# Optimization experiments

Measured on AMD Instinct MI355X. Metric: run time of the kernel, lower is better.

Reference implementation:

```python
import jax, jax.numpy as jnp
import numpy as np

B, T, D = 8, 16384, 128


def setup_inputs() -> dict:
    key = jax.random.key(0)
    ks = jax.random.split(key, 14)
    sc = lambda fan_in: 1.0 / np.sqrt(fan_in)
    x = jax.random.normal(ks[0], (B, T, D), jnp.float32)
    return {
        "x": x,
        # BindingField (scale 0): bind_key / bind_query Linear(D, D//2)
        "Wk": jax.random.normal(ks[1], (D, D // 2), jnp.float32) * sc(D),
        "bk": jnp.zeros((D // 2,), jnp.float32),
        "Wq": jax.random.normal(ks[2], (D, D // 2), jnp.float32) * sc(D),
        "bq": jnp.zeros((D // 2,), jnp.float32),
        # aggregator (scale 0): Linear(D,D) -> LayerNorm(D) -> ReLU -> Linear(D,D)
        "Wa1": jax.random.normal(ks[3], (D, D), jnp.float32) * sc(D),
        "ba1": jnp.zeros((D,), jnp.float32),
        "ln_g": jnp.ones((D,), jnp.float32),
        "ln_b": jnp.zeros((D,), jnp.float32),
        "Wa2": jax.random.normal(ks[4], (D, D), jnp.float32) * sc(D),
        "ba2": jnp.zeros((D,), jnp.float32),
        # downward_influence (scale 0): Linear(D,D)
        "Wd": jax.random.normal(ks[5], (D, D), jnp.float32) * sc(D),
        "bd": jnp.zeros((D,), jnp.float32),
    }


def reference(x, Wk, bk, Wq, bq, Wa1, ba1, ln_g, ln_b, Wa2, ba2, Wd, bd):
    Bn, Tn, Dn = x.shape
    BIND_THRESHOLD = 0.5
    LN_EPS = 1e-5

    # ---- BindingField: binding strength between adjacent tokens ----
    keys = x[:, :-1] @ Wk + bk                       # [B, T-1, D/2]
    queries = x[:, 1:] @ Wq + bq                     # [B, T-1, D/2]
    strength = jax.nn.sigmoid((keys * queries).sum(-1) / float(np.sqrt(Dn // 2)))
    bind = strength > BIND_THRESHOLD                 # [B, T-1]

    # chunk_starts: token 0 always starts; token t starts iff NOT bound to t-1
    chunk_starts = jnp.concatenate([jnp.ones((Bn, 1), bool), ~bind], axis=1)
    seg = jnp.cumsum(chunk_starts.astype(jnp.int32), axis=1) - 1  # [B, T] chunk id per token

    # ---- aggregate_chunks: ragged mean-pool via segment_sum (pad to T chunk slots) ----
    seg_flat = (seg + jnp.arange(Bn, dtype=jnp.int32)[:, None] * Tn).reshape(-1)
    sums = jax.ops.segment_sum(x.reshape(-1, Dn), seg_flat, num_segments=Bn * Tn)
    counts = jax.ops.segment_sum(jnp.ones((Bn * Tn,), x.dtype), seg_flat,
                                 num_segments=Bn * Tn)
    chunk_mean = (sums / jnp.maximum(counts, 1.0)[:, None]).reshape(Bn, Tn, Dn)

    # aggregator MLP: Linear -> LayerNorm -> ReLU -> Linear
    h = chunk_mean @ Wa1 + ba1
    mu = h.mean(-1, keepdims=True)
    var = ((h - mu) ** 2).mean(-1, keepdims=True)    # biased var, as torch LayerNorm
    h = (h - mu) * jax.lax.rsqrt(var + LN_EPS) * ln_g + ln_b
    agg = jax.nn.relu(h) @ Wa2 + ba2                 # [B, T(chunk slots), D]

    # ---- apply_downward_influence: broadcast chunk signal back to its tokens ----
    infl = agg @ Wd + bd                             # [B, T(chunks), D]
    gathered = jnp.take_along_axis(infl, seg[..., None].astype(jnp.int32), axis=1)
    gate = jax.nn.sigmoid(gathered)
    return x * gate + x
```

## Files before the change

kernel.cpp:

```cpp
#include <hip/hip_runtime.h>
#include <math.h>

#define BB 8
#define TT 16384
#define DD 128
#define DH 64
#define FCAP 32768
#define FMARGIN 0.05f

typedef _Float16 half8 __attribute__((ext_vector_type(8)));
typedef float f32x4 __attribute__((ext_vector_type(4)));

union H8 { half8 h; uint4 q; ushort us[8]; };

static __device__ __forceinline__ float4 ld4(const float* p) { return *(const float4*)p; }

static __device__ __forceinline__ uint pk2(float a, float b) {
    union { _Float16 f; ushort u; } A, B;
    A.f = (_Float16)a; B.f = (_Float16)b;
    return (uint)A.u | ((uint)B.u << 16);
}

static __device__ __forceinline__ void split8h(const float4 v0, const float4 v1,
                                               half8* xh, half8* xl)
{
    float f[8] = {v0.x, v0.y, v0.z, v0.w, v1.x, v1.y, v1.z, v1.w};
    half8 h, l;
    #pragma unroll
    for (int j = 0; j < 8; ++j) {
        _Float16 hv = (_Float16)f[j];
        h[j] = hv;
        l[j] = (_Float16)(f[j] - (float)hv);
    }
    *xh = h; *xl = l;
}

__global__ __launch_bounds__(64) void k_wprep(
    const float* __restrict__ Wa1, const float* __restrict__ Wa2,
    const float* __restrict__ Wd, const float* __restrict__ Wk,
    const float* __restrict__ Wq, ushort* __restrict__ wfm,
    ushort* __restrict__ wfb, int* __restrict__ fcnt)
{
    const int l  = threadIdx.x;
    const int nt = blockIdx.x & 7;
    const int kb = blockIdx.x >> 3;
    const int ly = blockIdx.y;
    if (ly == 0 && blockIdx.x == 0 && l == 0) *fcnt = 0;
    const int n  = nt * 16 + (l & 15);
    const int k0 = kb * 32 + (l >> 4) * 8;
    H8 v;
    if (ly < 3) {
        const float* W = (ly == 0) ? Wa1 : (ly == 1) ? Wa2 : Wd;
        #pragma unroll
        for (int e = 0; e < 8; ++e) v.h[e] = (_Float16)W[(k0 + e) * DD + n];
        *(uint4*)(wfm + (size_t)(((ly * 8 + nt) * 4 + kb) * 64 + l) * 8) = v.q;
    } else {
        #pragma unroll
        for (int e = 0; e < 8; ++e) {
            float w = (n < 64) ? Wk[(k0 + e) * DH + n] : Wq[(k0 + e) * DH + n - 64];
            v.h[e] = (_Float16)w;
        }
        *(uint4*)(wfb + (size_t)((nt * 4 + kb) * 64 + l) * 8) = v.q;
    }
}

__global__ __launch_bounds__(256, 2) void k_bind(
    const float* __restrict__ x, const ushort* __restrict__ wfb,
    const float* __restrict__ bk, const float* __restrict__ bq,
    int* __restrict__ cstart, int* __restrict__ flist, int* __restrict__ fcnt)
{
    __shared__ uint4 Bs4[2048];
    __shared__ float bnd[4][64];
    const int b    = blockIdx.y;
    const int tb   = blockIdx.x * 64;
    const int tid  = threadIdx.x;
    const int wv   = tid >> 6;
    const int l    = tid & 63;
    const int lo16 = l & 15;
    const int g    = l >> 4;

    {
        const uint4* wsrc = (const uint4*)wfb;
        #pragma unroll
        for (int j = 0; j < 8; ++j) { int idx = tid + j * 256; Bs4[idx] = wsrc[idx]; }
    }

    const float* xrow = x + ((size_t)b * TT + tb + wv * 16 + lo16) * DD;
    half8 xh[4], xl[4];
    #pragma unroll
    for (int kb = 0; kb < 4; ++kb) {
        float4 v0 = ld4(xrow + kb * 32 + g * 8);
        float4 v1 = ld4(xrow + kb * 32 + g * 8 + 4);
        split8h(v0, v1, &xh[kb], &xl[kb]);
    }
    int r64 = tb + 64; if (r64 > TT - 1) r64 = TT - 1;
    const float* xq = x + ((size_t)b * TT + r64) * DD;
    half8 qh[4], ql[4];
    H8 z; z.q.x = z.q.y = z.q.z = z.q.w = 0u;
    #pragma unroll
    for (int kb = 0; kb < 4; ++kb) {
        qh[kb] = z.h; ql[kb] = z.h;
        if (lo16 == 0) {
            float4 v0 = ld4(xq + kb * 32 + g * 8);
            float4 v1 = ld4(xq + kb * 32 + g * 8 + 4);
            split8h(v0, v1, &qh[kb], &ql[kb]);
        }
    }

    f32x4 acc[8];
    #pragma unroll
    for (int nt = 0; nt < 8; ++nt) {
        int col = nt * 16 + lo16;
        float bias = (col < 64) ? bk[col] : bq[col - 64];
        acc[nt] = (f32x4){bias, bias, bias, bias};
    }
    f32x4 acc4;
    {
        float bias = bq[wv * 16 + lo16];
        acc4 = (f32x4){bias, bias, bias, bias};
    }

    __syncthreads();
    const ushort* Bs = (const ushort*)Bs4;
    const ushort* Bs_halo = Bs + (size_t)((4 + wv) * 4 * 64 + l) * 8;
    #pragma unroll
    for (int kb = 0; kb < 4; ++kb) {
        half8 bh[8];
        #pragma unroll
        for (int nt = 0; nt < 8; ++nt)
            bh[nt] = *(const half8*)(Bs + (size_t)((nt * 4 + kb) * 64 + l) * 8);
        #pragma unroll
        for (int nt = 0; nt < 8; ++nt) {
            acc[nt] = __builtin_amdgcn_mfma_f32_16x16x32_f16(xh[kb], bh[nt], acc[nt], 0, 0, 0);
            acc[nt] = __builtin_amdgcn_mfma_f32_16x16x32_f16(xl[kb], bh[nt], acc[nt], 0, 0, 0);
        }
        half8 bh4 = *(const half8*)(Bs_halo + (size_t)kb * 64 * 8);
        acc4 = __builtin_amdgcn_mfma_f32_16x16x32_f16(qh[kb], bh4, acc4, 0, 0, 0);
        acc4 = __builtin_amdgcn_mfma_f32_16x16x32_f16(ql[kb], bh4, acc4, 0, 0, 0);
    }

    if (l < 16) {
        if (wv > 0) {
            #pragma unroll
            for (int nt = 0; nt < 4; ++nt) bnd[wv - 1][nt * 16 + lo16] = acc[4 + nt][0];
        }
        bnd[3][wv * 16 + lo16] = acc4[0];
    }
    __syncthreads();

    float qn3[4];
    #pragma unroll
    for (int nt = 0; nt < 4; ++nt) qn3[nt] = __shfl_down(acc[4 + nt][0], 16);
    if (g == 3) {
        #pragma unroll
        for (int nt = 0; nt < 4; ++nt) qn3[nt] = bnd[wv][nt * 16 + lo16];
    }
    float s[4];
    #pragma unroll
    for (int i = 0; i < 3; ++i) {
        float t = 0.f;
        #pragma unroll
        for (int nt = 0; nt < 4; ++nt) t += acc[nt][i] * acc[4 + nt][i + 1];
        s[i] = t;
    }
    {
        float t = 0.f;
        #pragma unroll
        for (int nt = 0; nt < 4; ++nt) t += acc[nt][3] * qn3[nt];
        s[3] = t;
    }
    #pragma unroll
    for (int i = 0; i < 4; ++i) {
        #pragma unroll
        for (int m = 1; m < 16; m <<= 1) s[i] += __shfl_xor(s[i], m);
    }
    if (lo16 == 0) {
        #pragma unroll
        for (int i = 0; i < 4; ++i) {
            int t = tb + wv * 16 + g * 4 + i;
            if (t <= TT - 2) {
                cstart[b * TT + t + 1] = (s[i] > 0.f) ? 0 : 1;
                if (fabsf(s[i]) < FMARGIN) {
                    int pos = atomicAdd(fcnt, 1);
                    if (pos < FCAP) flist[pos] = b * TT + t;
                }
            }
        }
    }
    if (blockIdx.x == 0 && tid == 0) cstart[b * TT] = 1;
}

__global__ __launch_bounds__(256) void k_fixup(
    const float* __restrict__ x, const float* __restrict__ Wk, const float* __restrict__ bk,
    const float* __restrict__ Wq, const float* __restrict__ bq,
    const int* __restrict__ flist, const int* __restrict__ fcnt, int* __restrict__ cstart)
{
    const int n    = min(*fcnt, FCAP);
    const int wv   = (blockIdx.x * 256 + threadIdx.x) >> 6;
    const int lane = threadIdx.x & 63;
    const int nwv  = gridDim.x * 4;
    for (int i = wv; i < n; i += nwv) {
        int idx = flist[i];
        int b = idx >> 14;
        int t = idx & (TT - 1);
        const float* xt = x + ((size_t)b * TT + t) * DD;
        float K = bk[lane], Q = bq[lane];
        #pragma unroll 8
        for (int k = 0; k < DD; ++k) {
            K = fmaf(xt[k],      Wk[k * DH + lane], K);
            Q = fmaf(xt[DD + k], Wq[k * DH + lane], Q);
        }
        float p = K * Q;
        #pragma unroll
        for (int m = 1; m < 64; m <<= 1) p += __shfl_xor(p, m);
        if (lane == 0) cstart[b * TT + t + 1] = (p > 0.f) ? 0 : 1;
    }
}

__global__ __launch_bounds__(1024) void k_scan(const int* __restrict__ cstart,
    int* __restrict__ seg, int* __restrict__ cs, int* __restrict__ numC)
{
    __shared__ int wsum[16];
    const int b = blockIdx.x, tid = threadIdx.x;
    const int wv = tid >> 6, lane = tid & 63;
    const int base = b * TT + tid * 16;
    int v[16];
    #pragma unroll
    for (int i = 0; i < 4; ++i) {
        int4 q = *(const int4*)(cstart + base + i * 4);
        v[i * 4 + 0] = q.x; v[i * 4 + 1] = q.y; v[i * 4 + 2] = q.z; v[i * 4 + 3] = q.w;
    }
    int s[16]; int run = 0;
    #pragma unroll
    for (int i = 0; i < 16; ++i) { run += v[i]; s[i] = run; }
    int incl = run;
    #pragma unroll
    for (int off = 1; off < 64; off <<= 1) {
        int t = __shfl_up(incl, off);
        if (lane >= off) incl += t;
    }
    if (lane == 63) wsum[wv] = incl;
    __syncthreads();
    if (tid < 16) {
        int w = wsum[tid];
        #pragma unroll
        for (int off = 1; off < 16; off <<= 1) {
            int t = __shfl_up(w, off, 16);
            if (tid >= off) w += t;
        }
        wsum[tid] = w;
    }
    __syncthreads();
    const int excl = (wv ? wsum[wv - 1] : 0) + incl - run;
    #pragma unroll
    for (int i = 0; i < 16; ++i) {
        int sg = excl + s[i] - 1;
        seg[base + i] = sg;
        if (v[i]) cs[b * (TT + 1) + sg] = tid * 16 + i;
    }
    if (tid == 1023) {
        int tot = excl + run;
        numC[b] = tot;
        cs[b * (TT + 1) + tot] = TT;
    }
}

__device__ __forceinline__ void mlp_gemm(f32x4 acc[8], const uint4* Afr4,
    const ushort* Bs, int wv, int l)
{
    half8 af[4];
    #pragma unroll
    for (int kb = 0; kb < 4; ++kb)
        af[kb] = *(const half8*)((const char*)Afr4 + ((wv * 4 + kb) * 64 + l) * 16);
    #pragma unroll
    for (int kb = 0; kb < 4; ++kb) {
        half8 bh[8];
        #pragma unroll
        for (int nt = 0; nt < 8; ++nt)
            bh[nt] = *(const half8*)(Bs + (size_t)((nt * 4 + kb) * 64 + l) * 8);
        #pragma unroll
        for (int nt = 0; nt < 8; ++nt)
            acc[nt] = __builtin_amdgcn_mfma_f32_16x16x32_f16(af[kb], bh[nt], acc[nt], 0, 0, 0);
    }
}

__global__ __launch_bounds__(256, 2) void k_mlp(
    const float* __restrict__ x, const int* __restrict__ cs,
    const float* __restrict__ ba1, const float* __restrict__ ln_g, const float* __restrict__ ln_b,
    const float* __restrict__ ba2, const float* __restrict__ bd,
    const ushort* __restrict__ wfm, const int* __restrict__ numC, float* __restrict__ cm)
{
    __shared__ union {
        float Tok[64 * 132];
        struct { uint4 Afr[1024]; uint4 Bs[2048]; } fb;
    } sm;
    const int b  = blockIdx.y;
    const int nC = numC[b];
    const int c0 = blockIdx.x * 64;
    if (c0 >= nC) return;
    const int tid  = threadIdx.x;
    const int wv   = tid >> 6;
    const int l    = tid & 63;
    const int lo16 = l & 15;
    const int g    = l >> 4;
    const ushort* Bs = (const ushort*)sm.fb.Bs;
    const uint4* wsrc = (const uint4*)wfm;

    const int cbase = b * (TT + 1);
    const int T0 = cs[cbase + c0];
    const int cEnd = (c0 + 64 < nC) ? (c0 + 64) : nC;
    const int T1 = cs[cbase + cEnd];
    int t0r[8], t1r[8];
    #pragma unroll
    for (int ii = 0; ii < 8; ++ii) {
        int r = (tid + ii * 256) >> 5;
        int c = c0 + r;
        t0r[ii] = (c < nC) ? cs[cbase + c] : 0;
        t1r[ii] = (c < nC) ? cs[cbase + c + 1] : 0;
    }
    float4 vals[8];
    #pragma unroll
    for (int ii = 0; ii < 8; ++ii) vals[ii] = make_float4(0.f, 0.f, 0.f, 0.f);

    for (int tt = T0; tt < T1; tt += 64) {
        __syncthreads();
        const int tEnd = (tt + 64 < T1) ? (tt + 64) : T1;
        for (int j = tid; j < (tEnd - tt) * 32; j += 256) {
            int trow = j >> 5, c4 = (j & 31) * 4;
            *(float4*)&sm.Tok[trow * 132 + c4] =
                ld4(x + ((size_t)b * TT + tt + trow) * DD + c4);
        }
        __syncthreads();
        #pragma unroll
        for (int ii = 0; ii < 8; ++ii) {
            int c4 = ((tid + ii * 256) & 31) * 4;
            int lo = (t0r[ii] > tt)   ? t0r[ii] : tt;
            int hi = (t1r[ii] < tEnd) ? t1r[ii] : tEnd;
            for (int t = lo; t < hi; ++t) {
                const float* ap = &sm.Tok[(t - tt) * 132 + c4];
                vals[ii].x += ap[0]; vals[ii].y += ap[1];
                vals[ii].z += ap[2]; vals[ii].w += ap[3];
            }
        }
    }
    __syncthreads();

    #pragma unroll
    for (int ii = 0; ii < 8; ++ii) {
        int i = tid + ii * 256;
        int r = i >> 5, c4 = (i & 31) * 4;
        float4 sv = make_float4(0.f, 0.f, 0.f, 0.f);
        if (c0 + r < nC) {
            float inv = 1.f / (float)(t1r[ii] - t0r[ii]);
            sv.x = vals[ii].x * inv; sv.y = vals[ii].y * inv;
            sv.z = vals[ii].z * inv; sv.w = vals[ii].w * inv;
        }
        int frag = (r >> 4) * 4 + (c4 >> 5);
        int lanef = (r & 15) + (((c4 & 31) >> 3) * 16);
        uint2 pk = make_uint2(pk2(sv.x, sv.y), pk2(sv.z, sv.w));
        *(uint2*)((char*)sm.fb.Afr + frag * 1024 + lanef * 16 + (c4 & 7) * 2) = pk;
    }
    #pragma unroll
    for (int j = 0; j < 8; ++j) { int idx = tid + j * 256; sm.fb.Bs[idx] = wsrc[idx]; }
    __syncthreads();

    f32x4 acc[8];
    #pragma unroll
    for (int nt = 0; nt < 8; ++nt) {
        float bias = ba1[nt * 16 + lo16];
        acc[nt] = (f32x4){bias, bias, bias, bias};
    }
    mlp_gemm(acc, sm.fb.Afr, Bs, wv, l);

    float mu_[4], rs_[4];
    #pragma unroll
    for (int i = 0; i < 4; ++i) {
        float smv = 0.f;
        #pragma unroll
        for (int nt = 0; nt < 8; ++nt) smv += acc[nt][i];
        #pragma unroll
        for (int k = 1; k < 16; k <<= 1) smv += __shfl_xor(smv, k, 16);
        mu_[i] = smv * (1.f / 128.f);
        float vs = 0.f;
        #pragma unroll
        for (int nt = 0; nt < 8; ++nt) { float d = acc[nt][i] - mu_[i]; vs += d * d; }
        #pragma unroll
        for (int k = 1; k < 16; k <<= 1) vs += __shfl_xor(vs, k, 16);
        rs_[i] = rsqrtf(vs * (1.f / 128.f) + 1e-5f);
    }
    float gam[8], bet[8];
    #pragma unroll
    for (int nt = 0; nt < 8; ++nt) { gam[nt] = ln_g[nt * 16 + lo16]; bet[nt] = ln_b[nt * 16 + lo16]; }

    __syncthreads();
    #pragma unroll
    for (int nt = 0; nt < 8; ++nt) {
        int cw = nt * 16 + lo16;
        int frag = wv * 4 + (cw >> 5);
        int lnf  = (((cw & 31) >> 3) * 16);
        #pragma unroll
        for (int i = 0; i < 4; ++i) {
            float h = fmaf((acc[nt][i] - mu_[i]) * rs_[i], gam[nt], bet[nt]);
            union { _Float16 f; ushort u; } cv; cv.f = (_Float16)fmaxf(h, 0.f);
            *((ushort*)((char*)sm.fb.Afr + frag * 1024 + ((g * 4 + i) + lnf) * 16 + (cw & 7) * 2)) = cv.u;
        }
    }
    #pragma unroll
    for (int j = 0; j < 8; ++j) { int idx = tid + j * 256; sm.fb.Bs[idx] = wsrc[2048 + idx]; }
    __syncthreads();

    #pragma unroll
    for (int nt = 0; nt < 8; ++nt) {
        float bias = ba2[nt * 16 + lo16];
        acc[nt] = (f32x4){bias, bias, bias, bias};
    }
    mlp_gemm(acc, sm.fb.Afr, Bs, wv, l);
    __syncthreads();
    #pragma unroll
    for (int nt = 0; nt < 8; ++nt) {
        int cw = nt * 16 + lo16;
        int frag = wv * 4 + (cw >> 5);
        int lnf  = (((cw & 31) >> 3) * 16);
        #pragma unroll
        for (int i = 0; i < 4; ++i) {
            union { _Float16 f; ushort u; } cv; cv.f = (_Float16)acc[nt][i];
            *((ushort*)((char*)sm.fb.Afr + frag * 1024 + ((g * 4 + i) + lnf) * 16 + (cw & 7) * 2)) = cv.u;
        }
    }
    #pragma unroll
    for (int j = 0; j < 8; ++j) { int idx = tid + j * 256; sm.fb.Bs[idx] = wsrc[4096 + idx]; }
    __syncthreads();

    #pragma unroll
    for (int nt = 0; nt < 8; ++nt) {
        float bias = bd[nt * 16 + lo16];
        acc[nt] = (f32x4){bias, bias, bias, bias};
    }
    mlp_gemm(acc, sm.fb.Afr, Bs, wv, l);
    #pragma unroll
    for (int i = 0; i < 4; ++i) {
        int row = c0 + wv * 16 + g * 4 + i;
        if (row < nC) {
            float* dst = cm + ((size_t)b * TT + row) * DD + lo16;
            #pragma unroll
            for (int nt = 0; nt < 8; ++nt)
                dst[nt * 16] = 1.f / (1.f + __expf(-acc[nt][i]));
        }
    }
}

__global__ __launch_bounds__(256) void k_out(const float* __restrict__ x,
    const int* __restrict__ seg, const float* __restrict__ gate, float* __restrict__ out)
{
    const size_t idx = (size_t)blockIdx.x * 256 + threadIdx.x;
    const size_t tok = idx >> 5;
    const int d4 = (int)(idx & 31);
    const int b  = (int)(tok >> 14);
    const int sg = seg[tok];
    float4 gv = ld4(gate + (((size_t)b << 14) + sg) * DD + d4 * 4);
    float4 xv = ld4(x + tok * DD + (size_t)d4 * 4);
    float4 o;
    o.x = fmaf(xv.x, gv.x, xv.x);
    o.y = fmaf(xv.y, gv.y, xv.y);
    o.z = fmaf(xv.z, gv.z, xv.z);
    o.w = fmaf(xv.w, gv.w, xv.w);
    *(float4*)(out + idx * 4) = o;
}

extern "C" void kernel_launch(void* const* d_in, const int* in_sizes, int n_in,
                              void* d_out, int out_size, void* d_ws, size_t ws_size,
                              hipStream_t stream)
{
    (void)in_sizes; (void)n_in; (void)out_size; (void)ws_size;
    const float* x    = (const float*)d_in[0];
    const float* Wk   = (const float*)d_in[1];
    const float* bk   = (const float*)d_in[2];
    const float* Wq   = (const float*)d_in[3];
    const float* bq   = (const float*)d_in[4];
    const float* Wa1  = (const float*)d_in[5];
    const float* ba1  = (const float*)d_in[6];
    const float* ln_g = (const float*)d_in[7];
    const float* ln_b = (const float*)d_in[8];
    const float* Wa2  = (const float*)d_in[9];
    const float* ba2  = (const float*)d_in[10];
    const float* Wd   = (const float*)d_in[11];
    const float* bd   = (const float*)d_in[12];
    float* out = (float*)d_out;

    char* p = (char*)d_ws;
    float* cm    = (float*)p;   p += (size_t)BB * TT * DD * 4;
    int* seg     = (int*)p;     p += (size_t)BB * TT * 4;
    int* cs      = (int*)p;     p += (size_t)BB * (TT + 1) * 4;
    int* numC    = (int*)p;     p += 64;
    ushort* wfm  = (ushort*)p;  p += 3 * DD * DD * 2;
    ushort* wfb  = (ushort*)p;  p += DD * DD * 2;
    int* flist   = (int*)p;     p += (size_t)FCAP * 4;
    int* fcnt    = (int*)p;

    k_wprep<<<dim3(32, 4), 64, 0, stream>>>(Wa1, Wa2, Wd, Wk, Wq, wfm, wfb, fcnt);
    k_bind<<<dim3(256, BB), 256, 0, stream>>>(x, wfb, bk, bq, seg, flist, fcnt);
    k_fixup<<<dim3(256), 256, 0, stream>>>(x, Wk, bk, Wq, bq, flist, fcnt, seg);
    k_scan<<<dim3(BB), 1024, 0, stream>>>(seg, seg, cs, numC);
    k_mlp<<<dim3(TT / 64, BB), 256, 0, stream>>>(x, cs, ba1, ln_g, ln_b, ba2, bd, wfm, numC, cm);
    k_out<<<dim3(BB * TT * DD / (256 * 4)), 256, 0, stream>>>(x, seg, cm, out);
}
```

Baseline: 118.2 us.

## Split chunk mean-pooling out of the fused MLP kernel into its own kernel

The ragged mean-pool stage moves out of k_mlp into a separate k_meanp kernel that writes fp32 chunk means to the cm workspace. A new k_mlp3 reads those means back and runs the three MFMA GEMMs plus LayerNorm. The pooling kernel uses a smaller 32-row token staging tile and no GEMM register state, so it can reach higher occupancy for the memory-bound part. The cost is an extra kernel launch and a write plus re-read of the chunk means through global memory.

```diff
diff --git a/kernel.cpp b/kernel.cpp
--- a/kernel.cpp
+++ b/kernel.cpp
@@ -265,6 +265,67 @@
     }
 }
 
+__global__ __launch_bounds__(256) void k_meanp(const float* __restrict__ x,
+    const int* __restrict__ cs, const int* __restrict__ numC, float* __restrict__ cm)
+{
+    __shared__ float Tok[32 * 132];
+    const int b  = blockIdx.y;
+    const int nC = numC[b];
+    const int c0 = blockIdx.x * 64;
+    if (c0 >= nC) return;
+    const int tid = threadIdx.x;
+    const int cbase = b * (TT + 1);
+    const int T0 = cs[cbase + c0];
+    const int cEnd = (c0 + 64 < nC) ? (c0 + 64) : nC;
+    const int T1 = cs[cbase + cEnd];
+    int t0r[8], t1r[8];
+    #pragma unroll
+    for (int ii = 0; ii < 8; ++ii) {
+        int r = (tid + ii * 256) >> 5;
+        int c = c0 + r;
+        t0r[ii] = (c < nC) ? cs[cbase + c] : 0;
+        t1r[ii] = (c < nC) ? cs[cbase + c + 1] : 0;
+    }
+    float4 vals[8];
+    #pragma unroll
+    for (int ii = 0; ii < 8; ++ii) vals[ii] = make_float4(0.f, 0.f, 0.f, 0.f);
+
+    for (int tt = T0; tt < T1; tt += 32) {
+        __syncthreads();
+        const int tEnd = (tt + 32 < T1) ? (tt + 32) : T1;
+        for (int j = tid; j < (tEnd - tt) * 32; j += 256) {
+            int trow = j >> 5, c4 = (j & 31) * 4;
+            *(float4*)&Tok[trow * 132 + c4] =
+                ld4(x + ((size_t)b * TT + tt + trow) * DD + c4);
+        }
+        __syncthreads();
+        #pragma unroll
+        for (int ii = 0; ii < 8; ++ii) {
+            int c4 = ((tid + ii * 256) & 31) * 4;
+            int lo = (t0r[ii] > tt)   ? t0r[ii] : tt;
+            int hi = (t1r[ii] < tEnd) ? t1r[ii] : tEnd;
+            for (int t = lo; t < hi; ++t) {
+                const float* ap = &Tok[(t - tt) * 132 + c4];
+                vals[ii].x += ap[0]; vals[ii].y += ap[1];
+                vals[ii].z += ap[2]; vals[ii].w += ap[3];
+            }
+        }
+    }
+    #pragma unroll
+    for (int ii = 0; ii < 8; ++ii) {
+        int i = tid + ii * 256;
+        int r = i >> 5, c4 = (i & 31) * 4;
+        int c = c0 + r;
+        if (c < nC) {
+            float inv = 1.f / (float)(t1r[ii] - t0r[ii]);
+            float4 sv;
+            sv.x = vals[ii].x * inv; sv.y = vals[ii].y * inv;
+            sv.z = vals[ii].z * inv; sv.w = vals[ii].w * inv;
+            *(float4*)(cm + ((size_t)b * TT + c) * DD + c4) = sv;
+        }
+    }
+}
+
 __device__ __forceinline__ void mlp_gemm(f32x4 acc[8], const uint4* Afr4,
     const ushort* Bs, int wv, int l)
 {
@@ -284,16 +345,13 @@
     }
 }
 
-__global__ __launch_bounds__(256, 2) void k_mlp(
-    const float* __restrict__ x, const int* __restrict__ cs,
+__global__ __launch_bounds__(256, 2) void k_mlp3(
+    const int* __restrict__ cs,
     const float* __restrict__ ba1, const float* __restrict__ ln_g, const float* __restrict__ ln_b,
     const float* __restrict__ ba2, const float* __restrict__ bd,
     const ushort* __restrict__ wfm, const int* __restrict__ numC, float* __restrict__ cm)
 {
-    __shared__ union {
-        float Tok[64 * 132];
-        struct { uint4 Afr[1024]; uint4 Bs[2048]; } fb;
-    } sm;
+    __shared__ struct { uint4 Afr[1024]; uint4 Bs[2048]; } fb;
     const int b  = blockIdx.y;
     const int nC = numC[b];
     const int c0 = blockIdx.x * 64;
@@ -303,65 +361,24 @@
     const int l    = tid & 63;
     const int lo16 = l & 15;
     const int g    = l >> 4;
-    const ushort* Bs = (const ushort*)sm.fb.Bs;
+    const ushort* Bs = (const ushort*)fb.Bs;
     const uint4* wsrc = (const uint4*)wfm;
-
-    const int cbase = b * (TT + 1);
-    const int T0 = cs[cbase + c0];
-    const int cEnd = (c0 + 64 < nC) ? (c0 + 64) : nC;
-    const int T1 = cs[cbase + cEnd];
-    int t0r[8], t1r[8];
-    #pragma unroll
-    for (int ii = 0; ii < 8; ++ii) {
-        int r = (tid + ii * 256) >> 5;
-        int c = c0 + r;
-        t0r[ii] = (c < nC) ? cs[cbase + c] : 0;
-        t1r[ii] = (c < nC) ? cs[cbase + c + 1] : 0;
-    }
-    float4 vals[8];
-    #pragma unroll
-    for (int ii = 0; ii < 8; ++ii) vals[ii] = make_float4(0.f, 0.f, 0.f, 0.f);
-
-    for (int tt = T0; tt < T1; tt += 64) {
-        __syncthreads();
-        const int tEnd = (tt + 64 < T1) ? (tt + 64) : T1;
-        for (int j = tid; j < (tEnd - tt) * 32; j += 256) {
-            int trow = j >> 5, c4 = (j & 31) * 4;
-            *(float4*)&sm.Tok[trow * 132 + c4] =
-                ld4(x + ((size_t)b * TT + tt + trow) * DD + c4);
-        }
-        __syncthreads();
-        #pragma unroll
-        for (int ii = 0; ii < 8; ++ii) {
-            int c4 = ((tid + ii * 256) & 31) * 4;
-            int lo = (t0r[ii] > tt)   ? t0r[ii] : tt;
-            int hi = (t1r[ii] < tEnd) ? t1r[ii] : tEnd;
-            for (int t = lo; t < hi; ++t) {
-                const float* ap = &sm.Tok[(t - tt) * 132 + c4];
-                vals[ii].x += ap[0]; vals[ii].y += ap[1];
-                vals[ii].z += ap[2]; vals[ii].w += ap[3];
-            }
-        }
-    }
-    __syncthreads();
+    (void)cs;
+
+    #pragma unroll
+    for (int j = 0; j < 8; ++j) { int idx = tid + j * 256; fb.Bs[idx] = wsrc[idx]; }
 
     #pragma unroll
     for (int ii = 0; ii < 8; ++ii) {
         int i = tid + ii * 256;
         int r = i >> 5, c4 = (i & 31) * 4;
         float4 sv = make_float4(0.f, 0.f, 0.f, 0.f);
-        if (c0 + r < nC) {
-            float inv = 1.f / (float)(t1r[ii] - t0r[ii]);
-            sv.x = vals[ii].x * inv; sv.y = vals[ii].y * inv;
-            sv.z = vals[ii].z * inv; sv.w = vals[ii].w * inv;
-        }
+        if (c0 + r < nC) sv = ld4(cm + ((size_t)b * TT + c0 + r) * DD + c4);
         int frag = (r >> 4) * 4 + (c4 >> 5);
         int lanef = (r & 15) + (((c4 & 31) >> 3) * 16);
         uint2 pk = make_uint2(pk2(sv.x, sv.y), pk2(sv.z, sv.w));
-        *(uint2*)((char*)sm.fb.Afr + frag * 1024 + lanef * 16 + (c4 & 7) * 2) = pk;
-    }
-    #pragma unroll
-    for (int j = 0; j < 8; ++j) { int idx = tid + j * 256; sm.fb.Bs[idx] = wsrc[idx]; }
+        *(uint2*)((char*)fb.Afr + frag * 1024 + lanef * 16 + (c4 & 7) * 2) = pk;
+    }
     __syncthreads();
 
     f32x4 acc[8];
@@ -370,7 +387,7 @@
         float bias = ba1[nt * 16 + lo16];
         acc[nt] = (f32x4){bias, bias, bias, bias};
     }
-    mlp_gemm(acc, sm.fb.Afr, Bs, wv, l);
+    mlp_gemm(acc, fb.Afr, Bs, wv, l);
 
     float mu_[4], rs_[4];
     #pragma unroll
@@ -402,11 +419,11 @@
         for (int i = 0; i < 4; ++i) {
             float h = fmaf((acc[nt][i] - mu_[i]) * rs_[i], gam[nt], bet[nt]);
             union { _Float16 f; ushort u; } cv; cv.f = (_Float16)fmaxf(h, 0.f);
-            *((ushort*)((char*)sm.fb.Afr + frag * 1024 + ((g * 4 + i) + lnf) * 16 + (cw & 7) * 2)) = cv.u;
-        }
-    }
-    #pragma unroll
-    for (int j = 0; j < 8; ++j) { int idx = tid + j * 256; sm.fb.Bs[idx] = wsrc[2048 + idx]; }
+            *((ushort*)((char*)fb.Afr + frag * 1024 + ((g * 4 + i) + lnf) * 16 + (cw & 7) * 2)) = cv.u;
+        }
+    }
+    #pragma unroll
+    for (int j = 0; j < 8; ++j) { int idx = tid + j * 256; fb.Bs[idx] = wsrc[2048 + idx]; }
     __syncthreads();
 
     #pragma unroll
@@ -414,7 +431,7 @@
         float bias = ba2[nt * 16 + lo16];
         acc[nt] = (f32x4){bias, bias, bias, bias};
     }
-    mlp_gemm(acc, sm.fb.Afr, Bs, wv, l);
+    mlp_gemm(acc, fb.Afr, Bs, wv, l);
     __syncthreads();
     #pragma unroll
     for (int nt = 0; nt < 8; ++nt) {
@@ -424,11 +441,11 @@
         #pragma unroll
         for (int i = 0; i < 4; ++i) {
             union { _Float16 f; ushort u; } cv; cv.f = (_Float16)acc[nt][i];
-            *((ushort*)((char*)sm.fb.Afr + frag * 1024 + ((g * 4 + i) + lnf) * 16 + (cw & 7) * 2)) = cv.u;
-        }
-    }
-    #pragma unroll
-    for (int j = 0; j < 8; ++j) { int idx = tid + j * 256; sm.fb.Bs[idx] = wsrc[4096 + idx]; }
+            *((ushort*)((char*)fb.Afr + frag * 1024 + ((g * 4 + i) + lnf) * 16 + (cw & 7) * 2)) = cv.u;
+        }
+    }
+    #pragma unroll
+    for (int j = 0; j < 8; ++j) { int idx = tid + j * 256; fb.Bs[idx] = wsrc[4096 + idx]; }
     __syncthreads();
 
     #pragma unroll
@@ -436,7 +453,7 @@
         float bias = bd[nt * 16 + lo16];
         acc[nt] = (f32x4){bias, bias, bias, bias};
     }
-    mlp_gemm(acc, sm.fb.Afr, Bs, wv, l);
+    mlp_gemm(acc, fb.Afr, Bs, wv, l);
     #pragma unroll
     for (int i = 0; i < 4; ++i) {
         int row = c0 + wv * 16 + g * 4 + i;
@@ -501,6 +518,7 @@
     k_bind<<<dim3(256, BB), 256, 0, stream>>>(x, wfb, bk, bq, seg, flist, fcnt);
     k_fixup<<<dim3(256), 256, 0, stream>>>(x, Wk, bk, Wq, bq, flist, fcnt, seg);
     k_scan<<<dim3(BB), 1024, 0, stream>>>(seg, seg, cs, numC);
-    k_mlp<<<dim3(TT / 64, BB), 256, 0, stream>>>(x, cs, ba1, ln_g, ln_b, ba2, bd, wfm, numC, cm);
+    k_meanp<<<dim3(TT / 64, BB), 256, 0, stream>>>(x, cs, numC, cm);
+    k_mlp3<<<dim3(TT / 64, BB), 256, 0, stream>>>(cs, ba1, ln_g, ln_b, ba2, bd, wfm, numC, cm);
     k_out<<<dim3(BB * TT * DD / (256 * 4)), 256, 0, stream>>>(x, seg, cm, out);
 }
```

Result: slower. 124.9 us (+5.7%).

## Double-buffer token tiles via direct global-to-LDS loads in chunk mean pooling

Applied to the files above, without the earlier changes.

Replaces the synchronous 64-row register-staged load of token rows into shared memory with a 32-row double-buffered scheme. It uses global_load_lds to copy x directly into LDS and prefetches the next tile while the current one is being summed. The goal is to hide global-load latency and drop the register round trip. In exchange the tiles are smaller, there are more loop iterations, a vmcnt wait plus barrier runs on every iteration, and the row padding (stride 132 to 128) is removed, which may add LDS bank conflicts.

```diff
diff --git a/kernel.cpp b/kernel.cpp
--- a/kernel.cpp
+++ b/kernel.cpp
@@ -291,7 +291,7 @@
     const ushort* __restrict__ wfm, const int* __restrict__ numC, float* __restrict__ cm)
 {
     __shared__ union {
-        float Tok[64 * 132];
+        float Tok[2][32 * 128];
         struct { uint4 Afr[1024]; uint4 Bs[2048]; } fb;
     } sm;
     const int b  = blockIdx.y;
@@ -322,27 +322,54 @@
     #pragma unroll
     for (int ii = 0; ii < 8; ++ii) vals[ii] = make_float4(0.f, 0.f, 0.f, 0.f);
 
-    for (int tt = T0; tt < T1; tt += 64) {
+    {
+        const int n16 = ((T0 + 32 < T1) ? 32 : (T1 - T0)) * 32;
+        #pragma unroll
+        for (int j = 0; j < 4; ++j) {
+            int base16 = j * 256 + wv * 64;
+            if (base16 + l < n16) {
+                const float* gs = x + ((size_t)b * TT + T0) * DD + (size_t)(base16 + l) * 4;
+                __builtin_amdgcn_global_load_lds(
+                    (const __attribute__((address_space(1))) void*)gs,
+                    (__attribute__((address_space(3))) void*)&sm.Tok[0][base16 * 4],
+                    16, 0, 0);
+            }
+        }
+    }
+    int buf = 0;
+    for (int tt = T0; tt < T1; tt += 32) {
+        asm volatile("s_waitcnt vmcnt(0)" ::: "memory");
         __syncthreads();
-        const int tEnd = (tt + 64 < T1) ? (tt + 64) : T1;
-        for (int j = tid; j < (tEnd - tt) * 32; j += 256) {
-            int trow = j >> 5, c4 = (j & 31) * 4;
-            *(float4*)&sm.Tok[trow * 132 + c4] =
-                ld4(x + ((size_t)b * TT + tt + trow) * DD + c4);
-        }
-        __syncthreads();
+        const int tEnd = (tt + 32 < T1) ? (tt + 32) : T1;
+        if (tt + 32 < T1) {
+            const int nEnd = (tt + 64 < T1) ? (tt + 64) : T1;
+            const int n16 = (nEnd - (tt + 32)) * 32;
+            #pragma unroll
+            for (int j = 0; j < 4; ++j) {
+                int base16 = j * 256 + wv * 64;
+                if (base16 + l < n16) {
+                    const float* gs = x + ((size_t)b * TT + tt + 32) * DD + (size_t)(base16 + l) * 4;
+                    __builtin_amdgcn_global_load_lds(
+                        (const __attribute__((address_space(1))) void*)gs,
+                        (__attribute__((address_space(3))) void*)&sm.Tok[buf ^ 1][base16 * 4],
+                        16, 0, 0);
+                }
+            }
+        }
         #pragma unroll
         for (int ii = 0; ii < 8; ++ii) {
             int c4 = ((tid + ii * 256) & 31) * 4;
             int lo = (t0r[ii] > tt)   ? t0r[ii] : tt;
             int hi = (t1r[ii] < tEnd) ? t1r[ii] : tEnd;
             for (int t = lo; t < hi; ++t) {
-                const float* ap = &sm.Tok[(t - tt) * 132 + c4];
+                const float* ap = &sm.Tok[buf][(t - tt) * 128 + c4];
                 vals[ii].x += ap[0]; vals[ii].y += ap[1];
                 vals[ii].z += ap[2]; vals[ii].w += ap[3];
             }
         }
-    }
+        buf ^= 1;
+    }
+    asm volatile("s_waitcnt vmcnt(0)" ::: "memory");
     __syncthreads();
 
     #pragma unroll
```

Result: faster. 113.9 us (-3.7%).
